# Optimization experiments

Hardware: AMD Instinct MI355X
Metric: run time of the kernel (lower is better)

The kernel has to match this reference:

```python
import jax, jax.numpy as jnp
import numpy as np


def _gcn_conv(x, src, dst, num_nodes, W, b):
    """PyG GCNConv: add self-loops, symmetric normalization, scatter-add, bias."""
    h = x @ W  # [N, F_out]
    # degree over destination nodes (all edge weights are 1, incl. self-loops)
    deg = jax.ops.segment_sum(jnp.ones_like(dst, dtype=h.dtype), dst,
                              num_segments=num_nodes)
    deg_inv_sqrt = jnp.where(deg > 0, jax.lax.rsqrt(deg), 0.0)
    norm = deg_inv_sqrt[src] * deg_inv_sqrt[dst]  # [E+N]
    msg = h[src] * norm[:, None]                  # gather + scale
    out = jax.ops.segment_sum(msg, dst, num_segments=num_nodes)  # scatter-add
    return out + b


def setup_inputs() -> dict:
    key = jax.random.key(0)
    k_x, k_e, k_w1, k_w2 = jax.random.split(key, 4)
    N, E, F = 50000, 800000, 128
    x = jax.random.normal(k_x, (N, F), dtype=jnp.float32)
    edge_index = jax.random.randint(k_e, (2, E), 0, N, dtype=jnp.int64)
    scale = 1.0 / np.sqrt(F)
    W1 = jax.random.normal(k_w1, (F, F), dtype=jnp.float32) * scale
    b1 = jnp.zeros((F,), dtype=jnp.float32)
    W2 = jax.random.normal(k_w2, (F, F), dtype=jnp.float32) * scale
    b2 = jnp.zeros((F,), dtype=jnp.float32)
    return {"x": x, "edge_index": edge_index, "W1": W1, "b1": b1,
            "W2": W2, "b2": b2}


def reference(x, edge_index, W1, b1, W2, b2):
    num_nodes = x.shape[0]
    loops = jnp.arange(num_nodes, dtype=edge_index.dtype)
    src = jnp.concatenate([edge_index[0], loops])
    dst = jnp.concatenate([edge_index[1], loops])
    # layer 1: GCNConv -> Identity norm -> relu -> dropout(eval=identity)
    h = jax.nn.relu(_gcn_conv(x, src, dst, num_nodes, W1, b1))
    # layer 2 (last_activation=True, so relu again)
    out = jax.nn.relu(_gcn_conv(h, src, dst, num_nodes, W2, b2))
    return out
```

## Files before the change

### kernel.cpp

```cpp
#include <hip/hip_runtime.h>
#include <hip/hip_bf16.h>

#define CDIV(a,b) (((a)+(b)-1)/(b))

typedef __bf16 bf16x8 __attribute__((ext_vector_type(8)));
typedef float  f32x4  __attribute__((ext_vector_type(4)));

union Frag16 { uint4 u; bf16x8 f; unsigned short s[8]; };
union Pack8  { unsigned short s[4]; uint2 u; };

__device__ __forceinline__ unsigned short f2bf(float f) {
    unsigned u = __float_as_uint(f);
    return (unsigned short)((u + 0x7fff + ((u >> 16) & 1)) >> 16);
}
__device__ __forceinline__ float bf2f(unsigned short s) {
    return __uint_as_float(((unsigned)s) << 16);
}

__device__ __forceinline__ int load_src(const int* e, int f, int E, int i) {
    return f ? e[i] : e[2 * i];
}
__device__ __forceinline__ int load_dst(const int* e, int f, int E, int i) {
    return f ? e[E + i] : e[2 * (E + i)];
}

__global__ __launch_bounds__(256) void prep_kernel(const float* __restrict__ W1,
                                                   const float* __restrict__ W2,
                                                   unsigned short* __restrict__ Wf1h,
                                                   unsigned short* __restrict__ Wf1l,
                                                   unsigned short* __restrict__ Wf2h,
                                                   unsigned short* __restrict__ Wf2l,
                                                   const int* __restrict__ edges,
                                                   int* __restrict__ flag, int E,
                                                   int4* __restrict__ zero_base, int Z4) {
    int tid = threadIdx.x;
    if (blockIdx.x == 2) {
        if (tid == 0) *flag = 0;
        __syncthreads();
        int n = min(E, 4096);
        int found = 0;
        for (int j = tid; j < n; j += 256) found |= (edges[2 * j + 1] != 0);
        if (found) *flag = 1;
        return;
    }
    if (blockIdx.x >= 3) {
        int idx = (blockIdx.x - 3) * 256 + tid;
        if (idx < Z4) zero_base[idx] = make_int4(0, 0, 0, 0);
        return;
    }
    const float* W = (blockIdx.x == 0) ? W1 : W2;
    unsigned short* Wfh = (blockIdx.x == 0) ? Wf1h : Wf2h;
    unsigned short* Wfl = (blockIdx.x == 0) ? Wf1l : Wf2l;
    #pragma unroll
    for (int it = 0; it < 8; ++it) {
        int c = it * 256 + tid;
        int ntk = c >> 6;
        int lane = c & 63;
        int ks = ntk & 3;
        int ntile = ntk >> 2;
        int quad = lane >> 4, nlo = lane & 15;
        int n = ntile * 16 + nlo;
        Frag16 h, l;
        #pragma unroll
        for (int j = 0; j < 8; ++j) {
            float w = W[(ks * 32 + quad * 8 + j) * 128 + n];
            h.s[j] = f2bf(w);
            float rr = w - bf2f(h.s[j]);
            l.s[j] = f2bf(rr);
        }
        *(uint4*)(Wfh + (size_t)c * 8) = h.u;
        *(uint4*)(Wfl + (size_t)c * 8) = l.u;
    }
}

__device__ __forceinline__ void gemm_body(const float* __restrict__ X,
                                          const unsigned short* __restrict__ Wfh,
                                          const unsigned short* __restrict__ Wfl,
                                          unsigned short* __restrict__ out16,
                                          int N, int blk,
                                          unsigned short (*Xh)[136],
                                          unsigned short (*Xl)[136]) {
    int tid = threadIdx.x;
    int row0 = blk * 64;
    #pragma unroll
    for (int it = 0; it < 8; ++it) {
        int f = it * 256 + tid;
        int r = f >> 5, c4 = f & 31;
        float4 v = make_float4(0.f, 0.f, 0.f, 0.f);
        int gr = row0 + r;
        if (gr < N) v = *(const float4*)(X + (size_t)gr * 128 + c4 * 4);
        float vv[4] = {v.x, v.y, v.z, v.w};
        Pack8 h, l;
        #pragma unroll
        for (int j = 0; j < 4; ++j) {
            h.s[j] = f2bf(vv[j]);
            float rr = vv[j] - bf2f(h.s[j]);
            l.s[j] = f2bf(rr);
        }
        *(uint2*)(&Xh[r][c4 * 4]) = h.u;
        *(uint2*)(&Xl[r][c4 * 4]) = l.u;
    }
    __syncthreads();

    int lane = tid & 63;
    int wv = tid >> 6;
    int quad = lane >> 4, nlo = lane & 15;
    f32x4 acc[8];
    #pragma unroll
    for (int t = 0; t < 8; ++t) acc[t] = (f32x4){0.f, 0.f, 0.f, 0.f};

    #pragma unroll
    for (int ks = 0; ks < 4; ++ks) {
        int kcol = ks * 32 + quad * 8;
        Frag16 xh, xl;
        xh.u = *(const uint4*)(&Xh[wv * 16 + nlo][kcol]);
        xl.u = *(const uint4*)(&Xl[wv * 16 + nlo][kcol]);
        #pragma unroll
        for (int t = 0; t < 8; ++t) {
            size_t cidx = ((size_t)(t * 4 + ks) * 64 + lane) * 8;
            Frag16 wh, wl;
            wh.u = *(const uint4*)(Wfh + cidx);
            wl.u = *(const uint4*)(Wfl + cidx);
            acc[t] = __builtin_amdgcn_mfma_f32_16x16x32_bf16(xh.f, wh.f, acc[t], 0, 0, 0);
            acc[t] = __builtin_amdgcn_mfma_f32_16x16x32_bf16(xh.f, wl.f, acc[t], 0, 0, 0);
            acc[t] = __builtin_amdgcn_mfma_f32_16x16x32_bf16(xl.f, wh.f, acc[t], 0, 0, 0);
        }
    }
    #pragma unroll
    for (int rg = 0; rg < 4; ++rg) {
        int gr = row0 + wv * 16 + quad * 4 + rg;
        if (gr < N) {
            #pragma unroll
            for (int t = 0; t < 8; ++t)
                out16[(size_t)gr * 128 + t * 16 + nlo] = f2bf(acc[t][rg]);
        }
    }
}

__global__ __launch_bounds__(256) void fat_kernel(const float* __restrict__ X,
                                                  const unsigned short* __restrict__ Wfh,
                                                  const unsigned short* __restrict__ Wfl,
                                                  unsigned short* __restrict__ out16,
                                                  int N, int Ggemm,
                                                  const int* __restrict__ edges,
                                                  const int* __restrict__ flag,
                                                  int* __restrict__ counts_sh,
                                                  int* __restrict__ rank, int E) {
    __shared__ unsigned short Xh[64][136];
    __shared__ unsigned short Xl[64][136];
    if (blockIdx.x < (unsigned)Ggemm) {
        gemm_body(X, Wfh, Wfl, out16, N, blockIdx.x, Xh, Xl);
        return;
    }
    int e = (blockIdx.x - Ggemm) * 256 + threadIdx.x;
    if (e >= E) return;
    int f = *flag;
    int d = load_dst(edges, f, E, e);
    int s = blockIdx.x & 7;
    int r = atomicAdd(&counts_sh[s * N + d], 1);
    rank[e] = (r << 3) | s;
}

__global__ __launch_bounds__(256) void gemm_h1_kernel(const unsigned short* __restrict__ H1,
                                                      const unsigned short* __restrict__ Wfh,
                                                      const unsigned short* __restrict__ Wfl,
                                                      unsigned short* __restrict__ out16,
                                                      int N) {
    int tid = threadIdx.x;
    int lane = tid & 63, wv = tid >> 6;
    int quad = lane >> 4, nlo = lane & 15;
    int row0 = blockIdx.x * 64 + wv * 16;
    int arow = min(row0 + nlo, N - 1);
    Frag16 xa[4];
    #pragma unroll
    for (int ks = 0; ks < 4; ++ks)
        xa[ks].u = *(const uint4*)(H1 + (size_t)arow * 128 + ks * 32 + quad * 8);

    f32x4 acc[8];
    #pragma unroll
    for (int t = 0; t < 8; ++t) acc[t] = (f32x4){0.f, 0.f, 0.f, 0.f};

    #pragma unroll
    for (int ks = 0; ks < 4; ++ks) {
        #pragma unroll
        for (int t = 0; t < 8; ++t) {
            size_t cidx = ((size_t)(t * 4 + ks) * 64 + lane) * 8;
            Frag16 wh, wl;
            wh.u = *(const uint4*)(Wfh + cidx);
            wl.u = *(const uint4*)(Wfl + cidx);
            acc[t] = __builtin_amdgcn_mfma_f32_16x16x32_bf16(xa[ks].f, wh.f, acc[t], 0, 0, 0);
            acc[t] = __builtin_amdgcn_mfma_f32_16x16x32_bf16(xa[ks].f, wl.f, acc[t], 0, 0, 0);
        }
    }
    #pragma unroll
    for (int rg = 0; rg < 4; ++rg) {
        int gr = row0 + quad * 4 + rg;
        if (gr < N) {
            #pragma unroll
            for (int t = 0; t < 8; ++t)
                out16[(size_t)gr * 128 + t * 16 + nlo] = f2bf(acc[t][rg]);
        }
    }
}

__global__ __launch_bounds__(256) void merge_dis_kernel(int* __restrict__ counts_sh,
                                                        int* __restrict__ counts,
                                                        float* __restrict__ dis,
                                                        int* __restrict__ bsum, int N) {
    __shared__ int red[4];
    int tid = threadIdx.x;
    int bs = 0;
    #pragma unroll
    for (int j = 0; j < 4; ++j) {
        int d = blockIdx.x * 1024 + j * 256 + tid;
        if (d < N) {
            int run = 0;
            #pragma unroll
            for (int s = 0; s < 8; ++s) {
                int v = counts_sh[s * N + d];
                counts_sh[s * N + d] = run;
                run += v;
            }
            counts[d] = run;
            dis[d] = rsqrtf((float)(run + 1));
            bs += run;
        }
    }
    #pragma unroll
    for (int off = 32; off >= 1; off >>= 1) bs += __shfl_down(bs, off, 64);
    if ((tid & 63) == 0) red[tid >> 6] = bs;
    __syncthreads();
    if (tid == 0) bsum[blockIdx.x] = red[0] + red[1] + red[2] + red[3];
}

__global__ void scan2_kernel(const int* __restrict__ bsum, int* __restrict__ boff,
                             int B, int* __restrict__ row_ptr, int N, int E) {
    int lane = threadIdx.x;
    int carry = 0;
    for (int base = 0; base < B; base += 64) {
        int i = base + lane;
        int v = (i < B) ? bsum[i] : 0;
        int x = v;
        #pragma unroll
        for (int off = 1; off < 64; off <<= 1) {
            int t = __shfl_up(x, off, 64);
            if (lane >= off) x += t;
        }
        if (i < B) boff[i] = carry + x - v;
        carry += __shfl(x, 63, 64);
    }
    if (lane == 0) row_ptr[N] = E;
}

__global__ __launch_bounds__(256) void scan3_kernel(const int* __restrict__ counts,
                                                    const int* __restrict__ boff,
                                                    int* __restrict__ row_ptr, int N) {
    __shared__ int wsum[4];
    int tid = threadIdx.x;
    int lane = tid & 63, wv = tid >> 6;
    int base = blockIdx.x * 1024 + tid * 4;
    int c[4];
    #pragma unroll
    for (int j = 0; j < 4; ++j) c[j] = (base + j < N) ? counts[base + j] : 0;
    int tsum = c[0] + c[1] + c[2] + c[3];
    int x = tsum;
    #pragma unroll
    for (int off = 1; off < 64; off <<= 1) {
        int t = __shfl_up(x, off, 64);
        if (lane >= off) x += t;
    }
    int texcl = x - tsum;
    if (lane == 63) wsum[wv] = x;
    __syncthreads();
    int woff = 0;
    for (int w = 0; w < wv; ++w) woff += wsum[w];
    int off0 = boff[blockIdx.x] + woff + texcl;
    int run = 0;
    #pragma unroll
    for (int j = 0; j < 4; ++j) {
        if (base + j < N) row_ptr[base + j] = off0 + run;
        run += c[j];
    }
}

__global__ void fill_kernel(const int* __restrict__ edges, const int* __restrict__ flag,
                            const int* __restrict__ row_ptr, const int* __restrict__ rank,
                            const int* __restrict__ counts_sh,
                            const float* __restrict__ dis, int2* __restrict__ edata,
                            int E, int N) {
    int e = blockIdx.x * blockDim.x + threadIdx.x;
    if (e >= E) return;
    int f = *flag;
    int s = load_src(edges, f, E, e);
    int d = load_dst(edges, f, E, e);
    int rk = rank[e];
    int sh = rk & 7;
    int pos = row_ptr[d] + counts_sh[sh * N + d] + (rk >> 3);
    edata[pos] = make_int2(s, __float_as_int(dis[s]));
}

template <bool BF16OUT>
__global__ __launch_bounds__(256) void agg_kernel(const unsigned short* __restrict__ H16,
                                                  const int* __restrict__ row_ptr,
                                                  const int2* __restrict__ edata,
                                                  const float* __restrict__ dis,
                                                  const float* __restrict__ bias,
                                                  void* __restrict__ outp, int N) {
    int wid = (blockIdx.x * blockDim.x + threadIdx.x) >> 6;
    int lane = threadIdx.x & 63;
    if (wid >= N) return;
    const ushort2* H2 = (const ushort2*)H16;
    float dd = dis[wid];
    ushort2 hv = H2[(size_t)wid * 64 + lane];
    float wself = dd * dd;
    float2 acc = make_float2(bf2f(hv.x) * wself, bf2f(hv.y) * wself);
    int e0 = __builtin_amdgcn_readfirstlane(row_ptr[wid]);
    int e1 = __builtin_amdgcn_readfirstlane(row_ptr[wid + 1]);
    for (int e = e0; e < e1; e += 8) {
        int rem = e1 - e;
        int   sj[8];
        float wj[8];
        #pragma unroll
        for (int j = 0; j < 8; ++j) {
            bool valid = j < rem;
            int2 ed = edata[valid ? e + j : e];
            sj[j] = ed.x;
            wj[j] = valid ? __int_as_float(ed.y) * dd : 0.f;
        }
        ushort2 aj[8];
        #pragma unroll
        for (int j = 0; j < 8; ++j)
            aj[j] = H2[(size_t)sj[j] * 64 + lane];
        #pragma unroll
        for (int j = 0; j < 8; ++j) {
            acc.x += bf2f(aj[j].x) * wj[j];
            acc.y += bf2f(aj[j].y) * wj[j];
        }
    }
    float2 b = ((const float2*)bias)[lane];
    float ox = fmaxf(acc.x + b.x, 0.f);
    float oy = fmaxf(acc.y + b.y, 0.f);
    if (BF16OUT) {
        ushort2 o = make_ushort2(f2bf(ox), f2bf(oy));
        ((ushort2*)outp)[(size_t)wid * 64 + lane] = o;
    } else {
        ((float2*)outp)[(size_t)wid * 64 + lane] = make_float2(ox, oy);
    }
}

extern "C" void kernel_launch(void* const* d_in, const int* in_sizes, int n_in,
                              void* d_out, int out_size, void* d_ws, size_t ws_size,
                              hipStream_t stream) {
    const float* x    = (const float*)d_in[0];
    const int*  edges = (const int*)d_in[1];
    const float* W1   = (const float*)d_in[2];
    const float* b1   = (const float*)d_in[3];
    const float* W2   = (const float*)d_in[4];
    const float* b2   = (const float*)d_in[5];
    float* out = (float*)d_out;

    const int F = 128;
    const int N = in_sizes[0] / F;
    const int E = in_sizes[1] / 2;
    const int NB = CDIV(N, 1024);
    const int Ggemm = CDIV(N, 64);
    const int Gcount = CDIV(E, 256);

    #define AL4(v) (((v) + 3) & ~3)
    unsigned short* A16 = (unsigned short*)d_ws;
    unsigned short* H1  = A16 + (size_t)AL4(N * F);
    float* dis      = (float*)(H1 + (size_t)AL4(N * F));
    int*  counts    = (int*)(dis + AL4(N));
    int*  counts_sh = counts + AL4(N);
    int*  flag      = counts_sh + AL4(8 * N);
    int*  row_ptr   = flag + 4;
    int*  bsum      = row_ptr + AL4(N + 1);
    int*  boff      = bsum + 64;
    int*  rank      = boff + 64;
    int2* edata     = (int2*)(rank + AL4(E));
    unsigned short* Wf1h = (unsigned short*)(edata + E);
    unsigned short* Wf1l = Wf1h + 16384;
    unsigned short* Wf2h = Wf1l + 16384;
    unsigned short* Wf2l = Wf2h + 16384;

    const int Z4 = AL4(8 * N) / 4;
    const int Gprep = 3 + CDIV(Z4, 256);

    prep_kernel<<<Gprep, 256, 0, stream>>>(W1, W2, Wf1h, Wf1l, Wf2h, Wf2l,
                                           edges, flag, E, (int4*)counts_sh, Z4);
    fat_kernel<<<Ggemm + Gcount, 256, 0, stream>>>(x, Wf1h, Wf1l, A16, N, Ggemm,
                                                   edges, flag, counts_sh, rank, E);
    merge_dis_kernel<<<NB, 256, 0, stream>>>(counts_sh, counts, dis, bsum, N);
    scan2_kernel<<<1, 64, 0, stream>>>(bsum, boff, NB, row_ptr, N, E);
    scan3_kernel<<<NB, 256, 0, stream>>>(counts, boff, row_ptr, N);
    fill_kernel<<<Gcount, 256, 0, stream>>>(edges, flag, row_ptr, rank,
                                            counts_sh, dis, edata, E, N);

    agg_kernel<true><<<CDIV(N * 64, 256), 256, 0, stream>>>(A16, row_ptr, edata, dis, b1, H1, N);
    gemm_h1_kernel<<<CDIV(N, 64), 256, 0, stream>>>(H1, Wf2h, Wf2l, A16, N);
    agg_kernel<false><<<CDIV(N * 64, 256), 256, 0, stream>>>(A16, row_ptr, edata, dis, b2, out, N);
}
```

Baseline: 224.9 us.

## Bucket CSR edges by source range, fuse scan kernels, unroll aggregation by 16

The counting pass now assigns each edge to one of eight sub-buckets by source index (s >> 13) rather than by block ID. Each destination's edge list therefore comes out grouped by source range, which should improve cache locality of the H row gathers during aggregation. The single-block scan2 kernel is folded into scan3: each block re-scans the block sums with its first wave, which removes one launch but assumes at most 64 blocks. The aggregation loop now issues 16 gathers per iteration instead of 8 to raise memory-level parallelism, at the cost of more registers and more wasted loads on short rows.

```diff
diff --git a/kernel.cpp b/kernel.cpp
--- a/kernel.cpp
+++ b/kernel.cpp
@@ -156,9 +156,10 @@
     if (e >= E) return;
     int f = *flag;
     int d = load_dst(edges, f, E, e);
-    int s = blockIdx.x & 7;
-    int r = atomicAdd(&counts_sh[s * N + d], 1);
-    rank[e] = (r << 3) | s;
+    int s = load_src(edges, f, E, e);
+    int b = s >> 13;
+    int r = atomicAdd(&counts_sh[b * N + d], 1);
+    rank[e] = (r << 3) | b;
 }
 
 __global__ __launch_bounds__(256) void gemm_h1_kernel(const unsigned short* __restrict__ H1,
@@ -233,31 +234,25 @@
     if (tid == 0) bsum[blockIdx.x] = red[0] + red[1] + red[2] + red[3];
 }
 
-__global__ void scan2_kernel(const int* __restrict__ bsum, int* __restrict__ boff,
-                             int B, int* __restrict__ row_ptr, int N, int E) {
-    int lane = threadIdx.x;
-    int carry = 0;
-    for (int base = 0; base < B; base += 64) {
-        int i = base + lane;
-        int v = (i < B) ? bsum[i] : 0;
+__global__ __launch_bounds__(256) void scan3_kernel(const int* __restrict__ counts,
+                                                    const int* __restrict__ bsum,
+                                                    int* __restrict__ row_ptr,
+                                                    int N, int NB, int E) {
+    __shared__ int wsum[4];
+    __shared__ int bo;
+    int tid = threadIdx.x;
+    int lane = tid & 63, wv = tid >> 6;
+    if (wv == 0) {
+        int v = (lane < NB) ? bsum[lane] : 0;
         int x = v;
         #pragma unroll
         for (int off = 1; off < 64; off <<= 1) {
             int t = __shfl_up(x, off, 64);
             if (lane >= off) x += t;
         }
-        if (i < B) boff[i] = carry + x - v;
-        carry += __shfl(x, 63, 64);
-    }
-    if (lane == 0) row_ptr[N] = E;
-}
-
-__global__ __launch_bounds__(256) void scan3_kernel(const int* __restrict__ counts,
-                                                    const int* __restrict__ boff,
-                                                    int* __restrict__ row_ptr, int N) {
-    __shared__ int wsum[4];
-    int tid = threadIdx.x;
-    int lane = tid & 63, wv = tid >> 6;
+        if (lane == (int)blockIdx.x) bo = x - v;
+    }
+    if (tid == 0 && blockIdx.x == 0) row_ptr[N] = E;
     int base = blockIdx.x * 1024 + tid * 4;
     int c[4];
     #pragma unroll
@@ -274,7 +269,7 @@
     __syncthreads();
     int woff = 0;
     for (int w = 0; w < wv; ++w) woff += wsum[w];
-    int off0 = boff[blockIdx.x] + woff + texcl;
+    int off0 = bo + woff + texcl;
     int run = 0;
     #pragma unroll
     for (int j = 0; j < 4; ++j) {
@@ -294,8 +289,8 @@
     int s = load_src(edges, f, E, e);
     int d = load_dst(edges, f, E, e);
     int rk = rank[e];
-    int sh = rk & 7;
-    int pos = row_ptr[d] + counts_sh[sh * N + d] + (rk >> 3);
+    int b = rk & 7;
+    int pos = row_ptr[d] + counts_sh[b * N + d] + (rk >> 3);
     edata[pos] = make_int2(s, __float_as_int(dis[s]));
 }
 
@@ -316,23 +311,23 @@
     float2 acc = make_float2(bf2f(hv.x) * wself, bf2f(hv.y) * wself);
     int e0 = __builtin_amdgcn_readfirstlane(row_ptr[wid]);
     int e1 = __builtin_amdgcn_readfirstlane(row_ptr[wid + 1]);
-    for (int e = e0; e < e1; e += 8) {
+    for (int e = e0; e < e1; e += 16) {
         int rem = e1 - e;
-        int   sj[8];
-        float wj[8];
-        #pragma unroll
-        for (int j = 0; j < 8; ++j) {
+        int   sj[16];
+        float wj[16];
+        #pragma unroll
+        for (int j = 0; j < 16; ++j) {
             bool valid = j < rem;
             int2 ed = edata[valid ? e + j : e];
             sj[j] = ed.x;
             wj[j] = valid ? __int_as_float(ed.y) * dd : 0.f;
         }
-        ushort2 aj[8];
-        #pragma unroll
-        for (int j = 0; j < 8; ++j)
+        ushort2 aj[16];
+        #pragma unroll
+        for (int j = 0; j < 16; ++j)
             aj[j] = H2[(size_t)sj[j] * 64 + lane];
         #pragma unroll
-        for (int j = 0; j < 8; ++j) {
+        for (int j = 0; j < 16; ++j) {
             acc.x += bf2f(aj[j].x) * wj[j];
             acc.y += bf2f(aj[j].y) * wj[j];
         }
@@ -375,8 +370,7 @@
     int*  flag      = counts_sh + AL4(8 * N);
     int*  row_ptr   = flag + 4;
     int*  bsum      = row_ptr + AL4(N + 1);
-    int*  boff      = bsum + 64;
-    int*  rank      = boff + 64;
+    int*  rank      = bsum + 64;
     int2* edata     = (int2*)(rank + AL4(E));
     unsigned short* Wf1h = (unsigned short*)(edata + E);
     unsigned short* Wf1l = Wf1h + 16384;
@@ -391,8 +385,7 @@
     fat_kernel<<<Ggemm + Gcount, 256, 0, stream>>>(x, Wf1h, Wf1l, A16, N, Ggemm,
                                                    edges, flag, counts_sh, rank, E);
     merge_dis_kernel<<<NB, 256, 0, stream>>>(counts_sh, counts, dis, bsum, N);
-    scan2_kernel<<<1, 64, 0, stream>>>(bsum, boff, NB, row_ptr, N, E);
-    scan3_kernel<<<NB, 256, 0, stream>>>(counts, boff, row_ptr, N);
+    scan3_kernel<<<NB, 256, 0, stream>>>(counts, bsum, row_ptr, N, NB, E);
     fill_kernel<<<Gcount, 256, 0, stream>>>(edges, flag, row_ptr, rank,
                                             counts_sh, dis, edata, E, N);
 
```

After: 226.2 us. About the same (+0.6%).
